# Kernel optimization log

Measured on AMD Instinct MI355X. Metric: run time of the kernel, lower is better.

Reference implementation:

```python
import jax, jax.numpy as jnp
import numpy as np
from jax import lax

B, N, F_, K, C = 16, 64, 1024, 13, 2   # batch, channels, feat(time), conv kernel, classes
EPS_BN = 1e-5


def setup_inputs() -> dict:
    key = jax.random.key(0)
    ks = jax.random.split(key, 12)
    kf = 1.0 / np.sqrt(F_)   # torch uniform init bound for Linear(F,.) and w
    kn = 1.0 / np.sqrt(N)    # Conv1d(N,1,k=1) bound
    kk = 1.0 / np.sqrt(K)    # Conv1d(1,1,k=K) bound
    u = lambda k, shape, b: jax.random.uniform(k, shape, jnp.float32, -b, b)
    return {
        "x": jax.random.normal(ks[0], (B, N, F_), jnp.float32),
        "w": u(ks[1], (F_,), kf),
        "gin_W": u(ks[2], (F_, F_), kf),
        "gin_b": u(ks[3], (F_,), kf),
        "bn1_g": jnp.ones((N,), jnp.float32),
        "bn1_b": jnp.zeros((N,), jnp.float32),
        "lc_W": u(ks[4], (N,), kn),
        "lc_b": u(ks[5], (1,), kn),
        "conv_W": u(ks[6], (1, 1, K), kk),
        "conv_b": u(ks[7], (1,), kk),
        "bn2_g": jnp.ones((1,), jnp.float32),
        "bn2_b": jnp.zeros((1,), jnp.float32),
        "out_W": u(ks[8], (C, F_), kf),
        "out_b": u(ks[9], (C,), kf),
    }


def reference(x, w, gin_W, gin_b, bn1_g, bn1_b, lc_W, lc_b, conv_W, conv_b,
              bn2_g, bn2_b, out_W, out_b):
    # --- learned adjacency: weighted L1 pairwise score ---
    diff = jnp.abs(x[:, :, None, :] - x[:, None, :, :])        # [B,N,N,F] big intermediate
    s = jnp.einsum('bijf,f->bij', diff, w)                      # [B,N,N]
    s = -jax.nn.relu(s)
    adj = jax.nn.softmax(s, axis=1)                             # softmax over dim 1 (as torch)
    # --- GIN aggregation (eps=0): (adj + I) @ x, then Linear ---
    a = adj + jnp.eye(N, dtype=x.dtype)
    h = jnp.einsum('bij,bjf->bif', a, x)                        # [B,N,F]
    h = jnp.einsum('bif,of->bio', h, gin_W) + gin_b             # [B,N,F]
    # --- BatchNorm1d over channels (train-mode batch stats, biased var) ---
    m = h.mean(axis=(0, 2), keepdims=True)
    v = h.var(axis=(0, 2), keepdims=True)
    h = (h - m) / jnp.sqrt(v + EPS_BN) * bn1_g[None, :, None] + bn1_b[None, :, None]
    # --- Conv1d(N->1, k=1): channel mixing ---
    y = jnp.einsum('bnf,n->bf', h, lc_W) + lc_b                 # [B,F]
    # --- Conv1d(1->1, k=K, padding='same') ---
    y = lax.conv_general_dilated(y[:, None, :], conv_W, (1,), 'SAME') + conv_b[None, :, None]
    # --- BatchNorm1d(1) ---
    m2 = y.mean(axis=(0, 2), keepdims=True)
    v2 = y.var(axis=(0, 2), keepdims=True)
    y = (y - m2) / jnp.sqrt(v2 + EPS_BN) * bn2_g[None, :, None] + bn2_b[None, :, None]
    # --- head ---
    y = jax.nn.relu(y.reshape(B, F_))
    logits = y @ out_W.T + out_b                                # [B,C]
    return jax.nn.softmax(logits, axis=1), adj
```

## Files before the change

kernel.cpp:

```cpp
#include <hip/hip_runtime.h>
#include <hip/hip_bf16.h>


typedef __attribute__((ext_vector_type(8))) __bf16 bf16x8;
typedef __attribute__((ext_vector_type(4))) float f32x4;

__device__ __forceinline__ unsigned short f2bf(float f) {
  union { float f; unsigned int u; } v; v.f = f;
  unsigned int r = v.u + 0x7FFFu + ((v.u >> 16) & 1u);
  return (unsigned short)(r >> 16);
}

__global__ __launch_bounds__(256) void k1_spart_gemm(
    const float* __restrict__ x, const float* __restrict__ w,
    const float* __restrict__ gin_W,
    float* __restrict__ spart, float* __restrict__ gpart) {
  __shared__ __align__(16) union {
    struct { float xt[64 * 68]; float wt[64]; } s;
    struct { unsigned short A[128 * 72]; unsigned short B[128 * 72]; } g;
  } sm;
  int t = threadIdx.x, bid = blockIdx.x;

  if (bid < 256) {
    int b = bid >> 4, ft = bid & 15, f0 = ft * 64;
    for (int c = 0; c < 16; ++c) {
      int idx = c * 256 + t;
      int n = idx >> 6, f = idx & 63;
      sm.s.xt[n * 68 + f] = x[b * 65536 + n * 1024 + f0 + f];
    }
    if (t < 64) sm.s.wt[t] = w[f0 + t];
    __syncthreads();
    int i0 = (t >> 4) * 4, j0 = (t & 15) * 4;
    float acc[4][4];
#pragma unroll
    for (int ii = 0; ii < 4; ++ii)
#pragma unroll
      for (int jj = 0; jj < 4; ++jj) acc[ii][jj] = 0.f;
    for (int f = 0; f < 64; f += 4) {
      float4 wv = *reinterpret_cast<const float4*>(&sm.s.wt[f]);
      float4 av[4], bv[4];
#pragma unroll
      for (int ii = 0; ii < 4; ++ii) av[ii] = *reinterpret_cast<const float4*>(&sm.s.xt[(i0 + ii) * 68 + f]);
#pragma unroll
      for (int jj = 0; jj < 4; ++jj) bv[jj] = *reinterpret_cast<const float4*>(&sm.s.xt[(j0 + jj) * 68 + f]);
#pragma unroll
      for (int ii = 0; ii < 4; ++ii)
#pragma unroll
        for (int jj = 0; jj < 4; ++jj) {
          acc[ii][jj] += fabsf(av[ii].x - bv[jj].x) * wv.x
                       + fabsf(av[ii].y - bv[jj].y) * wv.y
                       + fabsf(av[ii].z - bv[jj].z) * wv.z
                       + fabsf(av[ii].w - bv[jj].w) * wv.w;
        }
    }
    float* out = spart + (size_t)bid * 4096;
#pragma unroll
    for (int ii = 0; ii < 4; ++ii)
#pragma unroll
      for (int jj = 0; jj < 4; ++jj)
        out[(i0 + ii) * 64 + (j0 + jj)] = acc[ii][jj];
    return;
  }

  int g = bid - 256;
  int xcd = g & 7, idx = g >> 3;
  int lt = idx & 7, slice = idx >> 3;
  int tr = 2 * (xcd & 3) + (lt >> 2);
  int tc = 4 * (xcd >> 2) + (lt & 3);
  int k0 = slice * 512;
  int wave = t >> 6, lane = t & 63;
  int wr = (wave >> 1) * 64, wc = (wave & 1) * 64;
  int lrow = lane & 15, kg = lane >> 4;
  f32x4 acc[4][4];
#pragma unroll
  for (int mi = 0; mi < 4; ++mi)
#pragma unroll
    for (int nj = 0; nj < 4; ++nj) acc[mi][nj] = f32x4{0.f, 0.f, 0.f, 0.f};

  for (int chunk = 0; chunk < 8; ++chunk) {
    int kc = k0 + chunk * 64;
#pragma unroll
    for (int u = 0; u < 8; ++u) {
      int idx4 = u * 256 + t;
      int row = idx4 >> 4, kq = idx4 & 15;
      float4 va = *reinterpret_cast<const float4*>(&x[(size_t)(tr * 128 + row) * 1024 + kc + kq * 4]);
      ushort4 ua; ua.x = f2bf(va.x); ua.y = f2bf(va.y); ua.z = f2bf(va.z); ua.w = f2bf(va.w);
      *reinterpret_cast<ushort4*>(&sm.g.A[row * 72 + kq * 4]) = ua;
      float4 vb = *reinterpret_cast<const float4*>(&gin_W[(size_t)(tc * 128 + row) * 1024 + kc + kq * 4]);
      ushort4 ub; ub.x = f2bf(vb.x); ub.y = f2bf(vb.y); ub.z = f2bf(vb.z); ub.w = f2bf(vb.w);
      *reinterpret_cast<ushort4*>(&sm.g.B[row * 72 + kq * 4]) = ub;
    }
    __syncthreads();
#pragma unroll
    for (int ks = 0; ks < 2; ++ks) {
      bf16x8 af[4], bf_[4];
#pragma unroll
      for (int mi = 0; mi < 4; ++mi)
        af[mi] = *reinterpret_cast<const bf16x8*>(&sm.g.A[(wr + mi * 16 + lrow) * 72 + ks * 32 + kg * 8]);
#pragma unroll
      for (int nj = 0; nj < 4; ++nj)
        bf_[nj] = *reinterpret_cast<const bf16x8*>(&sm.g.B[(wc + nj * 16 + lrow) * 72 + ks * 32 + kg * 8]);
#pragma unroll
      for (int mi = 0; mi < 4; ++mi)
#pragma unroll
        for (int nj = 0; nj < 4; ++nj)
          acc[mi][nj] = __builtin_amdgcn_mfma_f32_16x16x32_bf16(af[mi], bf_[nj], acc[mi][nj], 0, 0, 0);
    }
    __syncthreads();
  }
  float* gp = gpart + (size_t)slice * (1024u * 1024u);
#pragma unroll
  for (int mi = 0; mi < 4; ++mi) {
    int row = tr * 128 + wr + mi * 16 + kg * 4;
#pragma unroll
    for (int nj = 0; nj < 4; ++nj) {
      int col = tc * 128 + wc + nj * 16 + lrow;
#pragma unroll
      for (int r = 0; r < 4; ++r)
        gp[(size_t)(row + r) * 1024 + col] = acc[mi][nj][r];
    }
  }
}

__global__ __launch_bounds__(256) void k2_adj_h2(
    const float* __restrict__ spart, const float* __restrict__ gpart,
    const float* __restrict__ gin_b,
    float* __restrict__ dout, float* __restrict__ h2, float* __restrict__ part) {
  __shared__ float adjs[64 * 65];
  __shared__ float csum[256];
  __shared__ float cinv[64];
  __shared__ __align__(16) float gt[64 * 68];
  int t = threadIdx.x, bid = blockIdx.x;
  int xcd = bid & 7, local = bid >> 3;
  int b = (xcd << 1) | (local & 1);
  int ft = local >> 1;
  int f0 = ft * 64;
  {
    int i = t >> 4, fl = (t & 15) * 4;
#pragma unroll
    for (int c = 0; c < 4; ++c) {
      int row = c * 16 + i;
      const float* base = gpart + (size_t)(b * 64 + row) * 1024 + f0 + fl;
      float4 s0 = *reinterpret_cast<const float4*>(base);
      float4 s1 = *reinterpret_cast<const float4*>(base + (1u << 20));
      float4 g4;
      g4.x = s0.x + s1.x; g4.y = s0.y + s1.y;
      g4.z = s0.z + s1.z; g4.w = s0.w + s1.w;
      *reinterpret_cast<float4*>(&gt[row * 68 + fl]) = g4;
    }
  }
  int jl = t & 63, q = t >> 6;
  float v[16];
#pragma unroll
  for (int r = 0; r < 16; ++r) v[r] = 0.f;
  for (int ft2 = 0; ft2 < 16; ++ft2) {
    const float* p = spart + (size_t)(b * 16 + ft2) * 4096 + jl;
#pragma unroll
    for (int r = 0; r < 16; ++r) v[r] += p[(q * 16 + r) * 64];
  }
  float partsum = 0.f;
#pragma unroll
  for (int r = 0; r < 16; ++r) {
    float e = expf(-fmaxf(v[r], 0.f));
    adjs[(q * 16 + r) * 65 + jl] = e;
    partsum += e;
  }
  csum[q * 64 + jl] = partsum;
  __syncthreads();
  if (t < 64)
    cinv[t] = 1.f / (csum[t] + csum[64 + t] + csum[128 + t] + csum[192 + t]);
  __syncthreads();
  float ci = cinv[jl];
  float* doutAdj = dout + 32 + (size_t)b * 4096;
#pragma unroll
  for (int r = 0; r < 16; ++r) {
    float a = adjs[(q * 16 + r) * 65 + jl] * ci;
    adjs[(q * 16 + r) * 65 + jl] = a;
    if (ft == 0) doutAdj[(q * 16 + r) * 64 + jl] = a;
  }
  __syncthreads();
  int i0 = (t >> 4) * 4, fl = (t & 15) * 4;
  float4 gbv = *reinterpret_cast<const float4*>(&gin_b[f0 + fl]);
  float4 acc4[4];
#pragma unroll
  for (int ii = 0; ii < 4; ++ii)
    acc4[ii] = *reinterpret_cast<const float4*>(&gt[(i0 + ii) * 68 + fl]);
  for (int j = 0; j < 64; ++j) {
    float4 gv = *reinterpret_cast<const float4*>(&gt[j * 68 + fl]);
#pragma unroll
    for (int ii = 0; ii < 4; ++ii) {
      float a = adjs[(i0 + ii) * 65 + j];
      acc4[ii].x += a * gv.x; acc4[ii].y += a * gv.y;
      acc4[ii].z += a * gv.z; acc4[ii].w += a * gv.w;
    }
  }
  float rs[4], rq[4];
#pragma unroll
  for (int ii = 0; ii < 4; ++ii) {
    acc4[ii].x += gbv.x; acc4[ii].y += gbv.y; acc4[ii].z += gbv.z; acc4[ii].w += gbv.w;
    *reinterpret_cast<float4*>(&h2[(size_t)(b * 64 + i0 + ii) * 1024 + f0 + fl]) = acc4[ii];
    rs[ii] = (acc4[ii].x + acc4[ii].y) + (acc4[ii].z + acc4[ii].w);
    rq[ii] = (acc4[ii].x * acc4[ii].x + acc4[ii].y * acc4[ii].y)
           + (acc4[ii].z * acc4[ii].z + acc4[ii].w * acc4[ii].w);
  }
#pragma unroll
  for (int m = 1; m < 16; m <<= 1) {
#pragma unroll
    for (int r = 0; r < 4; ++r) {
      rs[r] += __shfl_xor(rs[r], m, 64);
      rq[r] += __shfl_xor(rq[r], m, 64);
    }
  }
  if ((t & 15) == 0) {
    float* pp = part + (size_t)(b * 16 + ft) * 128;
#pragma unroll
    for (int r = 0; r < 4; ++r) {
      int n = i0 + r;
      pp[2 * n]     = rs[r];
      pp[2 * n + 1] = rq[r];
    }
  }
}

__global__ __launch_bounds__(256) void k3_y(
    const float* __restrict__ h2, const float* __restrict__ part,
    const float* __restrict__ lc_W, const float* __restrict__ lc_b,
    const float* __restrict__ bn1_g, const float* __restrict__ bn1_b,
    const float* __restrict__ conv_W, const float* __restrict__ conv_b,
    float* __restrict__ y2, float* __restrict__ bn2part) {
  __shared__ float redp[2][128];
  __shared__ float cls[64], dds[64];
  __shared__ float yloc[268];
  __shared__ float red[256], red2[256];
  __shared__ float c0s;
  int t = threadIdx.x, bid = blockIdx.x;
  int b = ((bid & 7) << 1) | ((bid >> 3) & 1);
  int fq = bid >> 4;
  int f0 = fq * 256;
  {
    int k = t & 127, h = t >> 7;
    float s = 0.f;
    const float* pp = part + (size_t)h * 128 * 128 + k;
    for (int p = 0; p < 128; ++p) s += pp[(size_t)p * 128];
    redp[h][k] = s;
  }
  __syncthreads();
  if (t < 64) {
    float sum = redp[0][2 * t] + redp[1][2 * t];
    float sq  = redp[0][2 * t + 1] + redp[1][2 * t + 1];
    float m = sum * (1.f / 16384.f);
    float var = sq * (1.f / 16384.f) - m * m;
    float inv = 1.f / sqrtf(var + 1e-5f);
    float g = bn1_g[t], be = bn1_b[t], lw = lc_W[t];
    cls[t] = lw * g * inv;
    dds[t] = lw * (be - m * inv * g);
  }
  __syncthreads();
  if (t == 0) {
    float s = 0.f;
    for (int n = 0; n < 64; ++n) s += dds[n];
    c0s = s + lc_b[0];
  }
  __syncthreads();
  float c0 = c0s;
  for (int idx = t; idx < 268; idx += 256) {
    int f = f0 - 6 + idx;
    float acc = 0.f;
    if (f >= 0 && f < 1024) {
      acc = c0;
      const float* col = h2 + (size_t)(b * 64) * 1024 + f;
      for (int n = 0; n < 64; ++n) acc += cls[n] * col[(size_t)n * 1024];
    }
    yloc[idx] = acc;
  }
  __syncthreads();
  float cw[13];
#pragma unroll
  for (int k = 0; k < 13; ++k) cw[k] = conv_W[k];
  float vv = conv_b[0];
#pragma unroll
  for (int k = 0; k < 13; ++k) vv += yloc[t + k] * cw[k];
  y2[b * 1024 + f0 + t] = vv;
  red[t] = vv; red2[t] = vv * vv;
  __syncthreads();
  for (int off = 128; off > 0; off >>= 1) {
    if (t < off) { red[t] += red[t + off]; red2[t] += red2[t + off]; }
    __syncthreads();
  }
  if (t == 0) {
    int dchunk = b * 4 + fq;
    bn2part[2 * dchunk] = red[0]; bn2part[2 * dchunk + 1] = red2[0];
  }
}

__global__ __launch_bounds__(256) void k4_head(
    const float* __restrict__ y2, const float* __restrict__ bn2part,
    const float* __restrict__ bn2_g, const float* __restrict__ bn2_b,
    const float* __restrict__ out_W, const float* __restrict__ out_b,
    float* __restrict__ dout) {
  int t = threadIdx.x;
  float S = 0.f, S2 = 0.f;
  for (int i = 0; i < 64; ++i) { S += bn2part[2 * i]; S2 += bn2part[2 * i + 1]; }
  float m2 = S * (1.f / 16384.f);
  float inv2 = 1.f / sqrtf(S2 * (1.f / 16384.f) - m2 * m2 + 1e-5f);
  float g2 = bn2_g[0] * inv2, be2 = bn2_b[0];
  int b = t >> 4, seg = t & 15;
  const float4* yv = reinterpret_cast<const float4*>(&y2[b * 1024 + seg * 64]);
  const float4* w0 = reinterpret_cast<const float4*>(&out_W[seg * 64]);
  const float4* w1 = reinterpret_cast<const float4*>(&out_W[1024 + seg * 64]);
  float a0 = 0.f, a1 = 0.f;
#pragma unroll 4
  for (int u = 0; u < 16; ++u) {
    float4 y4 = yv[u], c0 = w0[u], c1 = w1[u];
    float vx = fmaxf((y4.x - m2) * g2 + be2, 0.f);
    float vy = fmaxf((y4.y - m2) * g2 + be2, 0.f);
    float vz = fmaxf((y4.z - m2) * g2 + be2, 0.f);
    float vw = fmaxf((y4.w - m2) * g2 + be2, 0.f);
    a0 += vx * c0.x + vy * c0.y + vz * c0.z + vw * c0.w;
    a1 += vx * c1.x + vy * c1.y + vz * c1.z + vw * c1.w;
  }
  __shared__ float r0[256], r1[256];
  r0[t] = a0; r1[t] = a1;
  __syncthreads();
  for (int off = 8; off > 0; off >>= 1) {
    if (seg < off) { r0[t] += r0[t + off]; r1[t] += r1[t + off]; }
    __syncthreads();
  }
  if (seg == 0) {
    float l0 = r0[t] + out_b[0], l1 = r1[t] + out_b[1];
    float mx = fmaxf(l0, l1);
    float e0 = expf(l0 - mx), e1 = expf(l1 - mx);
    float inv = 1.f / (e0 + e1);
    dout[b * 2 + 0] = e0 * inv;
    dout[b * 2 + 1] = e1 * inv;
  }
}

extern "C" void kernel_launch(void* const* d_in, const int* in_sizes, int n_in,
                              void* d_out, int out_size, void* d_ws, size_t ws_size,
                              hipStream_t stream) {
  (void)in_sizes; (void)n_in; (void)out_size; (void)ws_size;
  const float* x      = (const float*)d_in[0];
  const float* w      = (const float*)d_in[1];
  const float* gin_W  = (const float*)d_in[2];
  const float* gin_b  = (const float*)d_in[3];
  const float* bn1_g  = (const float*)d_in[4];
  const float* bn1_b  = (const float*)d_in[5];
  const float* lc_W   = (const float*)d_in[6];
  const float* lc_b   = (const float*)d_in[7];
  const float* conv_W = (const float*)d_in[8];
  const float* conv_b = (const float*)d_in[9];
  const float* bn2_g  = (const float*)d_in[10];
  const float* bn2_b  = (const float*)d_in[11];
  const float* out_W  = (const float*)d_in[12];
  const float* out_b  = (const float*)d_in[13];
  float* dout = (float*)d_out;

  char* ws = (char*)d_ws;
  float* spart   = (float*)ws;
  float* h2      = (float*)(ws + (4u << 20));
  float* gpart   = (float*)(ws + (8u << 20));
  float* part    = (float*)(ws + (16u << 20));
  float* y2      = (float*)(ws + (16u << 20) + (128u << 10));
  float* bn2part = (float*)(ws + (16u << 20) + (192u << 10));

  k1_spart_gemm<<<dim3(384), dim3(256), 0, stream>>>(x, w, gin_W, spart, gpart);
  k2_adj_h2    <<<dim3(256), dim3(256), 0, stream>>>(spart, gpart, gin_b, dout, h2, part);
  k3_y         <<<dim3(64),  dim3(256), 0, stream>>>(h2, part, lc_W, lc_b, bn1_g, bn1_b,
                                                     conv_W, conv_b, y2, bn2part);
  k4_head      <<<dim3(1),   dim3(256), 0, stream>>>(y2, bn2part, bn2_g, bn2_b, out_W, out_b, dout);
}
```

Before: 68.91 us.

## Fuse head into k3 via last-block atomic ticket and use packed bf16 conversion

Merges the single-block head kernel into the k3 kernel: every block bumps an atomic counter after writing its partials, and the last block to arrive computes the BN2, linear head and softmax. This is meant to remove one kernel launch and its inter-kernel gap. A memset of the counter is added to the stream, which is itself an extra operation. It also replaces the manual float-to-bf16 rounding with packed __float22bfloat162_rn conversions in the GEMM staging loop.

```diff
diff --git a/kernel.cpp b/kernel.cpp
--- a/kernel.cpp
+++ b/kernel.cpp
@@ -5,10 +5,11 @@
 typedef __attribute__((ext_vector_type(8))) __bf16 bf16x8;
 typedef __attribute__((ext_vector_type(4))) float f32x4;
 
-__device__ __forceinline__ unsigned short f2bf(float f) {
-  union { float f; unsigned int u; } v; v.f = f;
-  unsigned int r = v.u + 0x7FFFu + ((v.u >> 16) & 1u);
-  return (unsigned short)(r >> 16);
+__device__ __forceinline__ uint2 cvt4_bf16(float4 v) {
+  union { __hip_bfloat162 h; unsigned int u; } a, b;
+  a.h = __float22bfloat162_rn(make_float2(v.x, v.y));
+  b.h = __float22bfloat162_rn(make_float2(v.z, v.w));
+  return make_uint2(a.u, b.u);
 }
 
 __global__ __launch_bounds__(256) void k1_spart_gemm(
@@ -84,11 +85,9 @@
       int idx4 = u * 256 + t;
       int row = idx4 >> 4, kq = idx4 & 15;
       float4 va = *reinterpret_cast<const float4*>(&x[(size_t)(tr * 128 + row) * 1024 + kc + kq * 4]);
-      ushort4 ua; ua.x = f2bf(va.x); ua.y = f2bf(va.y); ua.z = f2bf(va.z); ua.w = f2bf(va.w);
-      *reinterpret_cast<ushort4*>(&sm.g.A[row * 72 + kq * 4]) = ua;
+      *reinterpret_cast<uint2*>(&sm.g.A[row * 72 + kq * 4]) = cvt4_bf16(va);
       float4 vb = *reinterpret_cast<const float4*>(&gin_W[(size_t)(tc * 128 + row) * 1024 + kc + kq * 4]);
-      ushort4 ub; ub.x = f2bf(vb.x); ub.y = f2bf(vb.y); ub.z = f2bf(vb.z); ub.w = f2bf(vb.w);
-      *reinterpret_cast<ushort4*>(&sm.g.B[row * 72 + kq * 4]) = ub;
+      *reinterpret_cast<uint2*>(&sm.g.B[row * 72 + kq * 4]) = cvt4_bf16(vb);
     }
     __syncthreads();
 #pragma unroll
@@ -222,17 +221,21 @@
   }
 }
 
-__global__ __launch_bounds__(256) void k3_y(
+__global__ __launch_bounds__(256) void k3_y_head(
     const float* __restrict__ h2, const float* __restrict__ part,
     const float* __restrict__ lc_W, const float* __restrict__ lc_b,
     const float* __restrict__ bn1_g, const float* __restrict__ bn1_b,
     const float* __restrict__ conv_W, const float* __restrict__ conv_b,
-    float* __restrict__ y2, float* __restrict__ bn2part) {
+    const float* __restrict__ bn2_g, const float* __restrict__ bn2_b,
+    const float* __restrict__ out_W, const float* __restrict__ out_b,
+    float* __restrict__ y2, float* __restrict__ bn2part,
+    float* __restrict__ dout, unsigned* __restrict__ bar) {
   __shared__ float redp[2][128];
   __shared__ float cls[64], dds[64];
   __shared__ float yloc[268];
   __shared__ float red[256], red2[256];
   __shared__ float c0s;
+  __shared__ unsigned tk;
   int t = threadIdx.x, bid = blockIdx.x;
   int b = ((bid & 7) << 1) | ((bid >> 3) & 1);
   int fq = bid >> 4;
@@ -291,48 +294,48 @@
     int dchunk = b * 4 + fq;
     bn2part[2 * dchunk] = red[0]; bn2part[2 * dchunk + 1] = red2[0];
   }
-}
-
-__global__ __launch_bounds__(256) void k4_head(
-    const float* __restrict__ y2, const float* __restrict__ bn2part,
-    const float* __restrict__ bn2_g, const float* __restrict__ bn2_b,
-    const float* __restrict__ out_W, const float* __restrict__ out_b,
-    float* __restrict__ dout) {
-  int t = threadIdx.x;
-  float S = 0.f, S2 = 0.f;
-  for (int i = 0; i < 64; ++i) { S += bn2part[2 * i]; S2 += bn2part[2 * i + 1]; }
-  float m2 = S * (1.f / 16384.f);
-  float inv2 = 1.f / sqrtf(S2 * (1.f / 16384.f) - m2 * m2 + 1e-5f);
-  float g2 = bn2_g[0] * inv2, be2 = bn2_b[0];
-  int b = t >> 4, seg = t & 15;
-  const float4* yv = reinterpret_cast<const float4*>(&y2[b * 1024 + seg * 64]);
-  const float4* w0 = reinterpret_cast<const float4*>(&out_W[seg * 64]);
-  const float4* w1 = reinterpret_cast<const float4*>(&out_W[1024 + seg * 64]);
-  float a0 = 0.f, a1 = 0.f;
+
+  __syncthreads();
+  if (t == 0) { __threadfence(); tk = atomicAdd(bar, 1u); }
+  __syncthreads();
+  if (tk != 63u) return;
+  __threadfence();
+
+  {
+    float S = 0.f, S2 = 0.f;
+    for (int i = 0; i < 64; ++i) { S += bn2part[2 * i]; S2 += bn2part[2 * i + 1]; }
+    float m2 = S * (1.f / 16384.f);
+    float inv2 = 1.f / sqrtf(S2 * (1.f / 16384.f) - m2 * m2 + 1e-5f);
+    float g2 = bn2_g[0] * inv2, be2 = bn2_b[0];
+    int hb = t >> 4, seg = t & 15;
+    const float4* yv = reinterpret_cast<const float4*>(&y2[hb * 1024 + seg * 64]);
+    const float4* w0 = reinterpret_cast<const float4*>(&out_W[seg * 64]);
+    const float4* w1 = reinterpret_cast<const float4*>(&out_W[1024 + seg * 64]);
+    float a0 = 0.f, a1 = 0.f;
 #pragma unroll 4
-  for (int u = 0; u < 16; ++u) {
-    float4 y4 = yv[u], c0 = w0[u], c1 = w1[u];
-    float vx = fmaxf((y4.x - m2) * g2 + be2, 0.f);
-    float vy = fmaxf((y4.y - m2) * g2 + be2, 0.f);
-    float vz = fmaxf((y4.z - m2) * g2 + be2, 0.f);
-    float vw = fmaxf((y4.w - m2) * g2 + be2, 0.f);
-    a0 += vx * c0.x + vy * c0.y + vz * c0.z + vw * c0.w;
-    a1 += vx * c1.x + vy * c1.y + vz * c1.z + vw * c1.w;
-  }
-  __shared__ float r0[256], r1[256];
-  r0[t] = a0; r1[t] = a1;
-  __syncthreads();
-  for (int off = 8; off > 0; off >>= 1) {
-    if (seg < off) { r0[t] += r0[t + off]; r1[t] += r1[t + off]; }
-    __syncthreads();
-  }
-  if (seg == 0) {
-    float l0 = r0[t] + out_b[0], l1 = r1[t] + out_b[1];
-    float mx = fmaxf(l0, l1);
-    float e0 = expf(l0 - mx), e1 = expf(l1 - mx);
-    float inv = 1.f / (e0 + e1);
-    dout[b * 2 + 0] = e0 * inv;
-    dout[b * 2 + 1] = e1 * inv;
+    for (int u = 0; u < 16; ++u) {
+      float4 y4 = yv[u], cc0 = w0[u], cc1 = w1[u];
+      float vx = fmaxf((y4.x - m2) * g2 + be2, 0.f);
+      float vy = fmaxf((y4.y - m2) * g2 + be2, 0.f);
+      float vz = fmaxf((y4.z - m2) * g2 + be2, 0.f);
+      float vw = fmaxf((y4.w - m2) * g2 + be2, 0.f);
+      a0 += vx * cc0.x + vy * cc0.y + vz * cc0.z + vw * cc0.w;
+      a1 += vx * cc1.x + vy * cc1.y + vz * cc1.z + vw * cc1.w;
+    }
+    red[t] = a0; red2[t] = a1;
+    __syncthreads();
+    for (int off = 8; off > 0; off >>= 1) {
+      if (seg < off) { red[t] += red[t + off]; red2[t] += red2[t + off]; }
+      __syncthreads();
+    }
+    if (seg == 0) {
+      float l0 = red[t] + out_b[0], l1 = red2[t] + out_b[1];
+      float mx = fmaxf(l0, l1);
+      float e0 = expf(l0 - mx), e1 = expf(l1 - mx);
+      float inv = 1.f / (e0 + e1);
+      dout[hb * 2 + 0] = e0 * inv;
+      dout[hb * 2 + 1] = e1 * inv;
+    }
   }
 }
 
@@ -363,10 +366,12 @@
   float* part    = (float*)(ws + (16u << 20));
   float* y2      = (float*)(ws + (16u << 20) + (128u << 10));
   float* bn2part = (float*)(ws + (16u << 20) + (192u << 10));
-
+  unsigned* bar  = (unsigned*)(ws + (16u << 20) + (193u << 10));
+
+  hipMemsetAsync(bar, 0, 64, stream);
   k1_spart_gemm<<<dim3(384), dim3(256), 0, stream>>>(x, w, gin_W, spart, gpart);
   k2_adj_h2    <<<dim3(256), dim3(256), 0, stream>>>(spart, gpart, gin_b, dout, h2, part);
-  k3_y         <<<dim3(64),  dim3(256), 0, stream>>>(h2, part, lc_W, lc_b, bn1_g, bn1_b,
-                                                     conv_W, conv_b, y2, bn2part);
-  k4_head      <<<dim3(1),   dim3(256), 0, stream>>>(y2, bn2part, bn2_g, bn2_b, out_W, out_b, dout);
-}
+  k3_y_head    <<<dim3(64),  dim3(256), 0, stream>>>(h2, part, lc_W, lc_b, bn1_g, bn1_b,
+                                                     conv_W, conv_b, bn2_g, bn2_b, out_W, out_b,
+                                                     y2, bn2part, dout, bar);
+}
```

New measurement: 74.74 us. 8.5% more time.
